# Kernel tuning notes

Measured on AMD Instinct MI355X. Metric: run time of the kernel, lower is better.

The kernel has to match this reference:

```python
import jax, jax.numpy as jnp
import numpy as np

# Constants hard-coded in Phi_r.forward / Prior_SPDE (dx=dy=dt=1, tau=1, Qs=I)
KAPPA = 0.33
GAMMA = 1.0
BETA = 25.0
DT = 1.0


def _apply_A(u, H11, H12, H22):
    """Anisotropic SPDE operator A u = kappa^2 u - div(H grad u).

    u: [B, T, Y, X] field; H11/H12/H22: [B, Y, X] diffusion tensor entries.
    Centered 9-point stencil, zero (Dirichlet) boundary via zero padding --
    this is the dense-grid equivalent of the sparse DiffOperator assembly.
    """
    up = jnp.pad(u, ((0, 0), (0, 0), (1, 1), (1, 1)))
    c = up[:, :, 1:-1, 1:-1]
    uxx = up[:, :, 1:-1, 2:] - 2.0 * c + up[:, :, 1:-1, :-2]
    uyy = up[:, :, 2:, 1:-1] - 2.0 * c + up[:, :, :-2, 1:-1]
    uxy = 0.25 * (up[:, :, 2:, 2:] - up[:, :, 2:, :-2]
                  - up[:, :, :-2, 2:] + up[:, :, :-2, :-2])
    div = (H11[:, None] * uxx + 2.0 * H12[:, None] * uxy
           + H22[:, None] * uyy)
    return (KAPPA * KAPPA) * u - div


def setup_inputs() -> dict:
    key = jax.random.key(0)
    state = jax.random.normal(key, (8, 9, 512, 512), dtype=jnp.float32)
    return {"state": state}


def reference(state):
    # state: [n_b, n_t+2, n_y, n_x]
    n_b, n_tp2, n_y, n_x = state.shape
    n_t = n_tp2 - 2
    x = state[:, :n_t]            # [B, T, Y, X]
    vx = state[:, n_t]            # [B, Y, X]
    vy = state[:, n_t + 1]

    # H = gamma*I + beta * v v^T per node
    H11 = GAMMA + BETA * vx * vx
    H12 = BETA * vx * vy
    H22 = GAMMA + BETA * vy * vy

    # Apply operator to every time slice at once; M = I + dt*A
    Ax = _apply_A(x, H11, H12, H22)   # [B, T, Y, X]
    Mx = x + DT * Ax

    sq = lambda a: jnp.sum(a * a, axis=(-2, -1))  # reduce spatial dims
    nx = sq(x)    # [B, T]
    nM = sq(Mx)   # [B, T]

    # Block-tridiagonal precision Q (tau=1 -> Qs_tilde = I):
    #   Q00 = A^T A + 0.05 I + I            -> ||A x0||^2 + 1.05 ||x0||^2
    #   Qii = M^T M + I  (1 <= i <= T-2)    -> ||M xi||^2 + ||xi||^2
    #   Q(T-1,T-1) = M^T M                  -> ||M x_{T-1}||^2
    #   Q(i,i+1) = -M, Q(i+1,i) = -M^T      -> -2 xi . (M x_{i+1})
    cross = jnp.sum(x[:, : n_t - 1] * Mx[:, 1:], axis=(-2, -1)).sum(axis=-1)
    q = (sq(Ax[:, 0]) + 1.05 * nx[:, 0]
         + nM[:, 1:].sum(axis=1)
         + nx[:, 1 : n_t - 1].sum(axis=1)
         - 2.0 * cross)
    return q  # [n_b] quadratic forms x^T Q x
```

## Files before the change

### kernel.cpp

```cpp
#include <hip/hip_runtime.h>

#define N 512
#define KAPPA2 0.1089f
#define GAMMA  1.0f
#define BETA   25.0f

__device__ __forceinline__ void loadspan10(const float* __restrict__ p, int lane,
                                           float s[10]) {
    const float4 A = *reinterpret_cast<const float4*>(p);
    const float4 B = *reinterpret_cast<const float4*>(p + 4);
    s[1] = A.x; s[2] = A.y; s[3] = A.z; s[4] = A.w;
    s[5] = B.x; s[6] = B.y; s[7] = B.z; s[8] = B.w;
    const float lw = __shfl_up(B.w, 1, 64);
    const float rx = __shfl_down(A.x, 1, 64);
    s[0] = (lane == 0)  ? 0.0f : lw;
    s[9] = (lane == 63) ? 0.0f : rx;
}

__device__ __forceinline__ void zero10(float s[10]) {
    #pragma unroll
    for (int j = 0; j < 10; ++j) s[j] = 0.0f;
}

__global__ __launch_bounds__(256) void phi_q_stage1(const float* __restrict__ state,
                                                    float* __restrict__ ws) {
    const int bid  = blockIdx.x;
    const int b    = bid & 7;
    const int yt   = bid >> 3;
    const int tid  = threadIdx.x;
    const int wid  = tid >> 6;
    const int lane = tid & 63;
    const int y    = yt * 4 + wid;

    const size_t slice  = (size_t)N * N;
    const float* base   = state + (size_t)b * 9 * slice;
    const size_t rowoff = (size_t)y * N + lane * 8;

    const float4 vxA = *reinterpret_cast<const float4*>(base + 7 * slice + rowoff);
    const float4 vxB = *reinterpret_cast<const float4*>(base + 7 * slice + rowoff + 4);
    const float4 vyA = *reinterpret_cast<const float4*>(base + 8 * slice + rowoff);
    const float4 vyB = *reinterpret_cast<const float4*>(base + 8 * slice + rowoff + 4);
    float H11[8], H12[8], H22[8];
    {
        const float vxs[8] = {vxA.x, vxA.y, vxA.z, vxA.w, vxB.x, vxB.y, vxB.z, vxB.w};
        const float vys[8] = {vyA.x, vyA.y, vyA.z, vyA.w, vyB.x, vyB.y, vyB.z, vyB.w};
        #pragma unroll
        for (int j = 0; j < 8; ++j) {
            H11[j] = GAMMA + BETA * vxs[j] * vxs[j];
            H12[j] = BETA * vxs[j] * vys[j];
            H22[j] = GAMMA + BETA * vys[j] * vys[j];
        }
    }

    const bool ym = (y > 0), yp = (y < N - 1);

    float q = 0.0f;
    float prevc[8];
    #pragma unroll
    for (int j = 0; j < 8; ++j) prevc[j] = 0.0f;

    #pragma unroll
    for (int t = 0; t < 7; ++t) {
        const float* u = base + (size_t)t * slice;
        float sm[10], sc[10], su[10];

        loadspan10(u + rowoff, lane, sc);
        if (ym) loadspan10(u + rowoff - N, lane, sm);
        else    zero10(sm);
        if (yp) loadspan10(u + rowoff + N, lane, su);
        else    zero10(su);

        #pragma unroll
        for (int j = 0; j < 8; ++j) {
            const float c   = sc[j + 1];
            const float uxx = sc[j] + sc[j + 2] - 2.0f * c;
            const float uyy = sm[j + 1] + su[j + 1] - 2.0f * c;
            const float uxy = 0.25f * (su[j + 2] - su[j] - sm[j + 2] + sm[j]);
            const float div = H11[j] * uxx + 2.0f * H12[j] * uxy + H22[j] * uyy;
            const float Ax  = KAPPA2 * c - div;
            const float Mx  = c + Ax;

            if (t == 0) {
                q += Ax * Ax + 1.05f * c * c;
            } else {
                q += Mx * Mx;
                if (t < 6) q += c * c;
                q -= 2.0f * prevc[j] * Mx;
            }
            prevc[j] = c;
        }
    }

    #pragma unroll
    for (int off = 32; off > 0; off >>= 1)
        q += __shfl_down(q, off, 64);

    __shared__ float sred[4];
    if (lane == 0) sred[wid] = q;
    __syncthreads();
    if (tid == 0) ws[bid] = sred[0] + sred[1] + sred[2] + sred[3];
}

__global__ __launch_bounds__(128) void phi_q_stage2(const float* __restrict__ ws,
                                                    float* __restrict__ out) {
    const int b = blockIdx.x;
    float v = ws[b + 8 * threadIdx.x];
    #pragma unroll
    for (int off = 32; off > 0; off >>= 1)
        v += __shfl_down(v, off, 64);

    __shared__ float sred[2];
    const int lane = threadIdx.x & 63;
    const int wid  = threadIdx.x >> 6;
    if (lane == 0) sred[wid] = v;
    __syncthreads();
    if (threadIdx.x == 0) out[b] = sred[0] + sred[1];
}

extern "C" void kernel_launch(void* const* d_in, const int* in_sizes, int n_in,
                              void* d_out, int out_size, void* d_ws, size_t ws_size,
                              hipStream_t stream) {
    const float* state = (const float*)d_in[0];
    float* out = (float*)d_out;
    float* ws  = (float*)d_ws;

    phi_q_stage1<<<1024, 256, 0, stream>>>(state, ws);
    phi_q_stage2<<<8, 128, 0, stream>>>(ws, out);
}
```

Measured before the change: 26.19 us.

## Parallelize over time slices: one wave per time step, one block per row

Work is now split so each block handles a single (batch,row) pair and each of its 7 wavefronts processes a different time slice, instead of one wave looping serially over all 7 time slices for one row. The previous-slice centre values for the cross term are reloaded directly from global memory rather than carried in registers. The diffusion tensor is recomputed inline per wave, and the second-stage reduction is widened to cover 4096 partial sums. This raises parallelism and memory-level concurrency at the cost of redundant vx/vy loads, an extra read of the previous slice per wave, and 4x more blocks.

```diff
diff --git a/kernel.cpp b/kernel.cpp
--- a/kernel.cpp
+++ b/kernel.cpp
@@ -22,72 +22,66 @@
     for (int j = 0; j < 10; ++j) s[j] = 0.0f;
 }
 
-__global__ __launch_bounds__(256) void phi_q_stage1(const float* __restrict__ state,
-                                                    float* __restrict__ ws) {
+__global__ __launch_bounds__(448, 6) void phi_q_stage1(const float* __restrict__ state,
+                                                       float* __restrict__ ws) {
     const int bid  = blockIdx.x;
     const int b    = bid & 7;
-    const int yt   = bid >> 3;
+    const int y    = bid >> 3;
     const int tid  = threadIdx.x;
-    const int wid  = tid >> 6;
+    const int w    = tid >> 6;
     const int lane = tid & 63;
-    const int y    = yt * 4 + wid;
 
     const size_t slice  = (size_t)N * N;
     const float* base   = state + (size_t)b * 9 * slice;
     const size_t rowoff = (size_t)y * N + lane * 8;
 
+    const bool ym = (y > 0), yp = (y < N - 1);
+
     const float4 vxA = *reinterpret_cast<const float4*>(base + 7 * slice + rowoff);
     const float4 vxB = *reinterpret_cast<const float4*>(base + 7 * slice + rowoff + 4);
     const float4 vyA = *reinterpret_cast<const float4*>(base + 8 * slice + rowoff);
     const float4 vyB = *reinterpret_cast<const float4*>(base + 8 * slice + rowoff + 4);
-    float H11[8], H12[8], H22[8];
-    {
-        const float vxs[8] = {vxA.x, vxA.y, vxA.z, vxA.w, vxB.x, vxB.y, vxB.z, vxB.w};
-        const float vys[8] = {vyA.x, vyA.y, vyA.z, vyA.w, vyB.x, vyB.y, vyB.z, vyB.w};
+    const float vxs[8] = {vxA.x, vxA.y, vxA.z, vxA.w, vxB.x, vxB.y, vxB.z, vxB.w};
+    const float vys[8] = {vyA.x, vyA.y, vyA.z, vyA.w, vyB.x, vyB.y, vyB.z, vyB.w};
+
+    const float* u = base + (size_t)w * slice;
+    float sm[10], sc[10], su[10];
+    loadspan10(u + rowoff, lane, sc);
+    if (ym) loadspan10(u + rowoff - N, lane, sm);
+    else    zero10(sm);
+    if (yp) loadspan10(u + rowoff + N, lane, su);
+    else    zero10(su);
+
+    float xp8[8];
+    if (w > 0) {
+        const float* up = u - slice;
+        const float4 XA = *reinterpret_cast<const float4*>(up + rowoff);
+        const float4 XB = *reinterpret_cast<const float4*>(up + rowoff + 4);
+        xp8[0] = XA.x; xp8[1] = XA.y; xp8[2] = XA.z; xp8[3] = XA.w;
+        xp8[4] = XB.x; xp8[5] = XB.y; xp8[6] = XB.z; xp8[7] = XB.w;
+    } else {
         #pragma unroll
-        for (int j = 0; j < 8; ++j) {
-            H11[j] = GAMMA + BETA * vxs[j] * vxs[j];
-            H12[j] = BETA * vxs[j] * vys[j];
-            H22[j] = GAMMA + BETA * vys[j] * vys[j];
-        }
+        for (int j = 0; j < 8; ++j) xp8[j] = 0.0f;
     }
 
-    const bool ym = (y > 0), yp = (y < N - 1);
-
     float q = 0.0f;
-    float prevc[8];
     #pragma unroll
-    for (int j = 0; j < 8; ++j) prevc[j] = 0.0f;
-
-    #pragma unroll
-    for (int t = 0; t < 7; ++t) {
-        const float* u = base + (size_t)t * slice;
-        float sm[10], sc[10], su[10];
-
-        loadspan10(u + rowoff, lane, sc);
-        if (ym) loadspan10(u + rowoff - N, lane, sm);
-        else    zero10(sm);
-        if (yp) loadspan10(u + rowoff + N, lane, su);
-        else    zero10(su);
-
-        #pragma unroll
-        for (int j = 0; j < 8; ++j) {
-            const float c   = sc[j + 1];
-            const float uxx = sc[j] + sc[j + 2] - 2.0f * c;
-            const float uyy = sm[j + 1] + su[j + 1] - 2.0f * c;
-            const float uxy = 0.25f * (su[j + 2] - su[j] - sm[j + 2] + sm[j]);
-            const float div = H11[j] * uxx + 2.0f * H12[j] * uxy + H22[j] * uyy;
-            const float Ax  = KAPPA2 * c - div;
-            const float Mx  = c + Ax;
-
-            if (t == 0) {
-                q += Ax * Ax + 1.05f * c * c;
-            } else {
-                q += Mx * Mx;
-                if (t < 6) q += c * c;
-                q -= 2.0f * prevc[j] * Mx;
-            }
-            prevc[j] = c;
+    for (int j = 0; j < 8; ++j) {
+        const float c   = sc[j + 1];
+        const float uxx = sc[j] + sc[j + 2] - 2.0f * c;
+        const float uyy = sm[j + 1] + su[j + 1] - 2.0f * c;
+        const float uxy = 0.25f * (su[j + 2] - su[j] - sm[j + 2] + sm[j]);
+        const float vx = vxs[j], vy = vys[j];
+        const float div = (GAMMA + BETA * vx * vx) * uxx
+                        + (2.0f * BETA * vx * vy) * uxy
+                        + (GAMMA + BETA * vy * vy) * uyy;
+        const float Ax  = KAPPA2 * c - div;
+        if (w == 0) {
+            q += Ax * Ax + 1.05f * c * c;
+        } else {
+            const float Mx = c + Ax;
+            q += Mx * Mx - 2.0f * xp8[j] * Mx;
+            if (w < 6) q += c * c;
         }
     }
 
@@ -95,26 +89,29 @@
     for (int off = 32; off > 0; off >>= 1)
         q += __shfl_down(q, off, 64);
 
-    __shared__ float sred[4];
-    if (lane == 0) sred[wid] = q;
+    __shared__ float sred[7];
+    if (lane == 0) sred[w] = q;
     __syncthreads();
-    if (tid == 0) ws[bid] = sred[0] + sred[1] + sred[2] + sred[3];
+    if (tid == 0) {
+        ws[bid] = sred[0] + sred[1] + sred[2] + sred[3]
+                + sred[4] + sred[5] + sred[6];
+    }
 }
 
-__global__ __launch_bounds__(128) void phi_q_stage2(const float* __restrict__ ws,
+__global__ __launch_bounds__(256) void phi_q_stage2(const float* __restrict__ ws,
                                                     float* __restrict__ out) {
     const int b = blockIdx.x;
-    float v = ws[b + 8 * threadIdx.x];
+    float v = ws[b + 8 * threadIdx.x] + ws[b + 8 * (threadIdx.x + 256)];
     #pragma unroll
     for (int off = 32; off > 0; off >>= 1)
         v += __shfl_down(v, off, 64);
 
-    __shared__ float sred[2];
+    __shared__ float sred[4];
     const int lane = threadIdx.x & 63;
     const int wid  = threadIdx.x >> 6;
     if (lane == 0) sred[wid] = v;
     __syncthreads();
-    if (threadIdx.x == 0) out[b] = sred[0] + sred[1];
+    if (threadIdx.x == 0) out[b] = sred[0] + sred[1] + sred[2] + sred[3];
 }
 
 extern "C" void kernel_launch(void* const* d_in, const int* in_sizes, int n_in,
@@ -124,6 +121,6 @@
     float* out = (float*)d_out;
     float* ws  = (float*)d_ws;
 
-    phi_q_stage1<<<1024, 256, 0, stream>>>(state, ws);
-    phi_q_stage2<<<8, 128, 0, stream>>>(ws, out);
+    phi_q_stage1<<<4096, 448, 0, stream>>>(state, ws);
+    phi_q_stage2<<<8, 256, 0, stream>>>(ws, out);
 }
```

Result: no change. 26.09 us (-0.4%).
